# Optimization experiments

Hardware: AMD Instinct MI355X
Metric: run time of the kernel (lower is better)

Reference implementation:

```python
import jax, jax.numpy as jnp
import numpy as np

B, H, W, D, K = 64, 32, 32, 64, 512


def setup_inputs() -> dict:
    key = jax.random.key(0)
    k1, k2 = jax.random.split(key)
    x = jax.random.normal(k1, (B, H, W, D), dtype=jnp.float32)
    # tf.random_uniform_initializer default: U(-0.05, 0.05)
    embeddings = jax.random.uniform(k2, (D, K), dtype=jnp.float32,
                                    minval=-0.05, maxval=0.05)
    return {"x": x, "embeddings": embeddings}


def reference(x, embeddings):
    # embeddings: [D, K] (columns are codebook vectors)
    d = embeddings.shape[0]
    flat = x.reshape(-1, d)  # [N, D]
    # squared L2 distance to each code: ||z||^2 + ||e||^2 - 2 z.e
    distances = (jnp.sum(flat * flat, axis=1, keepdims=True)
                 + jnp.sum(embeddings * embeddings, axis=0)
                 - 2.0 * flat @ embeddings)  # [N, K]
    encoding_indices = jnp.argmin(distances, axis=1)  # [N]
    # one-hot @ embeddings^T  ==  gather of codebook rows
    quantized = jnp.take(embeddings.T, encoding_indices, axis=0).reshape(x.shape)
    sg = jax.lax.stop_gradient
    commitment_loss = jnp.mean((sg(quantized) - x) ** 2)  # commitment_cost = 1
    codebook_loss = jnp.mean((quantized - sg(x)) ** 2)
    loss = commitment_loss + codebook_loss
    out = x + sg(quantized - x)  # straight-through estimator
    return out, loss
```

## Files before the change

### kernel.cpp

```cpp
#include <hip/hip_runtime.h>

#define NVEC 65536
#define DIM 64
#define KCODES 512
#define VPB 128
#define NBLK 512
#define ELS 2048.0f
#define INV_ELS (1.0f / 2048.0f)
#define BIAS 8.0f
#define GAP_THR 2.5e-4f

typedef _Float16 f16x8 __attribute__((ext_vector_type(8)));
typedef float    f32x4 __attribute__((ext_vector_type(4)));
typedef unsigned long long u64;

#define WS_EN   4
#define WS_EH   1024
#define WS_EL   (1024 + 16384)
#define WS_PART 33792
#define WS_EMBT 34816

__global__ __launch_bounds__(512, 1) void prep_kernel(const float* __restrict__ emb,
                                                      float* __restrict__ ws) {
    const int tid = threadIdx.x;
    const int b   = blockIdx.x;
    if (b == 0) {
        float s = 0.f;
#pragma unroll
        for (int d = 0; d < DIM; ++d) { float v = emb[d * KCODES + tid]; s = fmaf(v, v, s); }
        ws[WS_EN + tid] = s;
    } else if (b <= 8) {
        const int fl = (b - 1) * 512 + tid;
        const int ct = fl >> 7, s5 = (fl >> 6) & 1, l = fl & 63;
        const int k  = ct * 16 + (l & 15);
        const int d0 = s5 * 32 + (l >> 4) * 8;
        f16x8 eh, el;
#pragma unroll
        for (int e = 0; e < 8; ++e) {
            float v = emb[(d0 + e) * KCODES + k];
            _Float16 h = (_Float16)v;
            _Float16 l16 = (_Float16)((v - (float)h) * ELS);
            eh[e] = -(h + h);
            el[e] = -(l16 + l16);
        }
        ((f16x8*)(ws + WS_EH))[fl] = eh;
        ((f16x8*)(ws + WS_EL))[fl] = el;
    } else {
        __shared__ float tl[64][65];
        const int kt = b - 9;
        const int r  = tid >> 3;
        const int g  = tid & 7;
#pragma unroll
        for (int i = 0; i < 8; ++i)
            tl[r][g * 8 + i] = emb[r * KCODES + kt * 64 + g * 8 + i];
        __syncthreads();
#pragma unroll
        for (int i = 0; i < 8; ++i)
            ws[WS_EMBT + (kt * 64 + r) * 64 + g * 8 + i] = tl[g * 8 + i][r];
    }
}

__global__ __launch_bounds__(512, 2) void vq_kernel(const float* __restrict__ x,
                                                    const float* __restrict__ ws_ro,
                                                    float* __restrict__ out,
                                                    float* __restrict__ part) {
    __shared__ f16x8 zhS[VPB][8];
    __shared__ f16x8 zlS[VPB][8];
    __shared__ float enS8[KCODES];
    __shared__ int   cand[VPB][2];
    __shared__ float sdfm[VPB][2];
    __shared__ float exd[VPB][2];
    __shared__ int   bksel[VPB];
    __shared__ float swl[8];

    const int tid  = threadIdx.x;
    const int wid  = tid >> 6;
    const int lane = tid & 63;
    const size_t xbase = (size_t)blockIdx.x * VPB * DIM;

    enS8[tid] = ws_ro[WS_EN + tid] + BIAS;

    {
        const int v  = tid >> 2;
        const int d0 = (tid & 3) * 16;
        const float* xp = x + xbase + v * DIM + d0;
        float4 a = *(const float4*)(xp);
        float4 b = *(const float4*)(xp + 4);
        float4 c = *(const float4*)(xp + 8);
        float4 e = *(const float4*)(xp + 12);
        float t0[8] = {a.x, a.y, a.z, a.w, b.x, b.y, b.z, b.w};
        float t1[8] = {c.x, c.y, c.z, c.w, e.x, e.y, e.z, e.w};
        f16x8 h0, l0, h1, l1;
#pragma unroll
        for (int i = 0; i < 8; ++i) {
            _Float16 h = (_Float16)t0[i]; h0[i] = h; l0[i] = (_Float16)((t0[i] - (float)h) * ELS);
            _Float16 g = (_Float16)t1[i]; h1[i] = g; l1[i] = (_Float16)((t1[i] - (float)g) * ELS);
        }
        const int u0 = ((d0 >> 3))     ^ (v & 7);
        const int u1 = ((d0 >> 3) + 1) ^ (v & 7);
        zhS[v][u0] = h0; zhS[v][u1] = h1;
        zlS[v][u0] = l0; zlS[v][u1] = l1;
    }
    __syncthreads();

    const int vb  = wid * 16;
    const int col = lane & 15;
    const int g4  = lane >> 4;
    const int vA  = vb + col;
    const int sw  = vA & 7;
    f16x8 ah0 = zhS[vA][(g4)     ^ sw];
    f16x8 ah1 = zhS[vA][(4 + g4) ^ sw];
    f16x8 al0 = zlS[vA][(g4)     ^ sw];
    f16x8 al1 = zlS[vA][(4 + g4) ^ sw];

    const f16x8* ehp = (const f16x8*)(ws_ro + WS_EH);
    const f16x8* elp = (const f16x8*)(ws_ro + WS_EL);

    unsigned b1[4] = {~0u, ~0u, ~0u, ~0u};
    unsigned b2[4] = {~0u, ~0u, ~0u, ~0u};

    f16x8 Ah0 = ehp[lane],        Ah1 = ehp[64 + lane];
    f16x8 Al0 = elp[lane],        Al1 = elp[64 + lane];
    f16x8 Bh0 = ehp[128 + lane],  Bh1 = ehp[192 + lane];
    f16x8 Bl0 = elp[128 + lane],  Bl1 = elp[192 + lane];
    int onx = 256 + lane;

#define COMPUTE(T, H0, H1, L0, L1) { \
        const float enk8 = enS8[(T) * 16 + col]; \
        f32x4 acch  = {enk8, enk8, enk8, enk8}; \
        f32x4 accm1 = {0.f, 0.f, 0.f, 0.f}; \
        f32x4 accm2 = {0.f, 0.f, 0.f, 0.f}; \
        acch  = __builtin_amdgcn_mfma_f32_16x16x32_f16(ah0, H0, acch,  0, 0, 0); \
        acch  = __builtin_amdgcn_mfma_f32_16x16x32_f16(ah1, H1, acch,  0, 0, 0); \
        accm1 = __builtin_amdgcn_mfma_f32_16x16x32_f16(al0, H0, accm1, 0, 0, 0); \
        accm1 = __builtin_amdgcn_mfma_f32_16x16x32_f16(ah0, L0, accm1, 0, 0, 0); \
        accm2 = __builtin_amdgcn_mfma_f32_16x16x32_f16(al1, H1, accm2, 0, 0, 0); \
        accm2 = __builtin_amdgcn_mfma_f32_16x16x32_f16(ah1, L1, accm2, 0, 0, 0); \
        _Pragma("unroll") \
        for (int j = 0; j < 4; ++j) { \
            float scb = fmaf(accm1[j] + accm2[j], INV_ELS, acch[j]); \
            unsigned u = (__float_as_uint(scb) & 0xFFFFFFE0u) | (unsigned)(T); \
            b2[j] = min(b2[j], max(u, b1[j])); \
            b1[j] = min(b1[j], u); \
        } }

#pragma unroll 1
    for (int ct = 0; ct < 32; ct += 2) {
        COMPUTE(ct, Ah0, Ah1, Al0, Al1)
        Ah0 = ehp[onx]; Ah1 = ehp[onx + 64];
        Al0 = elp[onx]; Al1 = elp[onx + 64];
        COMPUTE(ct + 1, Bh0, Bh1, Bl0, Bl1)
        Bh0 = ehp[onx + 128]; Bh1 = ehp[onx + 192];
        Bl0 = elp[onx + 128]; Bl1 = elp[onx + 192];
        onx += 256;
    }
#undef COMPUTE

    u64 q1[4], q2[4];
#pragma unroll
    for (int j = 0; j < 4; ++j) {
        q1[j] = ((u64)(b1[j] & 0xFFFFFFE0u) << 32) | (unsigned)((b1[j] & 31u) * 16 + col);
        q2[j] = ((u64)(b2[j] & 0xFFFFFFE0u) << 32) | (unsigned)((b2[j] & 31u) * 16 + col);
    }
#pragma unroll
    for (int m = 1; m <= 8; m <<= 1) {
#pragma unroll
        for (int j = 0; j < 4; ++j) {
            u64 qa = __shfl_xor(q1[j], m);
            u64 qb = __shfl_xor(q2[j], m);
            u64 lo = q1[j] < qa ? q1[j] : qa;
            u64 hi = q1[j] < qa ? qa : q1[j];
            u64 s2 = q2[j] < qb ? q2[j] : qb;
            q1[j] = lo;
            q2[j] = hi < s2 ? hi : s2;
        }
    }
    {
        const int j = lane & 15;
        if (j < 4) {
            const int v = vb + g4 * 4 + j;
            u64 s1 = j == 0 ? q1[0] : j == 1 ? q1[1] : j == 2 ? q1[2] : q1[3];
            u64 s2 = j == 0 ? q2[0] : j == 1 ? q2[1] : j == 2 ? q2[2] : q2[3];
            sdfm[v][0] = __uint_as_float((unsigned)(s1 >> 32));
            sdfm[v][1] = __uint_as_float((unsigned)(s2 >> 32));
            cand[v][0] = (int)(s1 & 0x1FFu);
            cand[v][1] = (int)(s2 & 0x1FFu);
        }
    }
    __syncthreads();

    if (tid < 2 * VPB) {
        const int v = tid >> 1, cc = tid & 1;
        float res = sdfm[v][cc];
        if (sdfm[v][1] - sdfm[v][0] <= GAP_THR) {
            const int k = cand[v][cc];
            const float* xr = x + xbase + v * DIM;
            const float* er = ws_ro + WS_EMBT + k * 64;
            float zn = 0.f, dot = 0.f;
#pragma unroll
            for (int d = 0; d < DIM; ++d) {
                float xv = xr[d];
                zn  = fmaf(xv, xv, zn);
                dot = fmaf(xv, er[d], dot);
            }
            res = fmaf(-2.0f, dot, zn + ws_ro[WS_EN + k]);
        }
        exd[v][cc] = res;
    }
    __syncthreads();
    if (tid < VPB) {
        const int k0 = cand[tid][0], k1 = cand[tid][1];
        const float d0 = exd[tid][0], d1 = exd[tid][1];
        const bool take2 = (d1 < d0) || (d1 == d0 && k1 < k0);
        bksel[tid] = take2 ? k1 : k0;
    }
    __syncthreads();

    const int v16 = tid >> 2;
    const int j16 = (tid & 3) * 16;
    const int bk  = bksel[v16];
    const int gvec = blockIdx.x * VPB + v16;
    const float*  xg  = x + (size_t)gvec * DIM + j16;
    float*        og  = out + (size_t)gvec * DIM + j16;
    const float4* et4 = (const float4*)(ws_ro + WS_EMBT + bk * 64);

    float lossLocal = 0.f;
#pragma unroll
    for (int c = 0; c < 4; ++c) {
        float4 q  = et4[(tid & 3) * 4 + c];
        *(float4*)(og + c * 4) = q;
        float4 xa = *(const float4*)(xg + c * 4);
        float a;
        a = q.x - xa.x; lossLocal = fmaf(a, a, lossLocal);
        a = q.y - xa.y; lossLocal = fmaf(a, a, lossLocal);
        a = q.z - xa.z; lossLocal = fmaf(a, a, lossLocal);
        a = q.w - xa.w; lossLocal = fmaf(a, a, lossLocal);
    }

#pragma unroll
    for (int off = 32; off; off >>= 1) lossLocal += __shfl_down(lossLocal, off, 64);
    if (lane == 0) swl[wid] = lossLocal;
    __syncthreads();
    if (tid == 0) {
        float s = 0.f;
#pragma unroll
        for (int i = 0; i < 8; ++i) s += swl[i];
        part[WS_PART + blockIdx.x] = s;
    }
}

__global__ __launch_bounds__(256, 1) void finish_kernel(const float* __restrict__ part,
                                                        float* __restrict__ out) {
    __shared__ float sw[4];
    const int tid = threadIdx.x, lane = tid & 63, wid = tid >> 6;
    float s = part[WS_PART + tid] + part[WS_PART + tid + 256];
#pragma unroll
    for (int off = 32; off; off >>= 1) s += __shfl_down(s, off, 64);
    if (lane == 0) sw[wid] = s;
    __syncthreads();
    if (tid == 0) {
        float total = sw[0] + sw[1] + sw[2] + sw[3];
        out[(size_t)NVEC * DIM] = 2.0f * total / (float)((size_t)NVEC * DIM);
    }
}

extern "C" void kernel_launch(void* const* d_in, const int* in_sizes, int n_in,
                              void* d_out, int out_size, void* d_ws, size_t ws_size,
                              hipStream_t stream) {
    const float* x   = (const float*)d_in[0];
    const float* emb = (const float*)d_in[1];
    float* out = (float*)d_out;
    float* ws  = (float*)d_ws;

    prep_kernel<<<dim3(17), dim3(512), 0, stream>>>(emb, ws);
    vq_kernel<<<dim3(NBLK), dim3(512), 0, stream>>>(x, ws, out, ws);
    finish_kernel<<<dim3(1), dim3(256), 0, stream>>>(ws, out);
}
```

Before: 39.11 us.

## Split codebook across wave pairs, each wave scoring 32 vectors

Each wave now handles 32 vectors against half of the codebook instead of 16 vectors against all 512 codes. Every loaded codebook fragment therefore feeds twice as many MFMAs, and the per-wave loop is half as long. A shared-memory merge step then combines the top-2 candidates from the two halves. Launch bounds are raised to 4 blocks per SM to target higher occupancy, at the cost of more registers per wave for the doubled fragments and accumulators, an extra barrier, and more shared memory.

```diff
diff --git a/kernel.cpp b/kernel.cpp
--- a/kernel.cpp
+++ b/kernel.cpp
@@ -60,13 +60,15 @@
     }
 }
 
-__global__ __launch_bounds__(512, 2) void vq_kernel(const float* __restrict__ x,
+__global__ __launch_bounds__(512, 4) void vq_kernel(const float* __restrict__ x,
                                                     const float* __restrict__ ws_ro,
                                                     float* __restrict__ out,
                                                     float* __restrict__ part) {
     __shared__ f16x8 zhS[VPB][8];
     __shared__ f16x8 zlS[VPB][8];
     __shared__ float enS8[KCODES];
+    __shared__ float sdf1[2][VPB], sdf2[2][VPB];
+    __shared__ int   k1a[2][VPB],  k2a[2][VPB];
     __shared__ int   cand[VPB][2];
     __shared__ float sdfm[VPB][2];
     __shared__ float exd[VPB][2];
@@ -103,89 +105,130 @@
     }
     __syncthreads();
 
-    const int vb  = wid * 16;
-    const int col = lane & 15;
-    const int g4  = lane >> 4;
-    const int vA  = vb + col;
-    const int sw  = vA & 7;
-    f16x8 ah0 = zhS[vA][(g4)     ^ sw];
-    f16x8 ah1 = zhS[vA][(4 + g4) ^ sw];
-    f16x8 al0 = zlS[vA][(g4)     ^ sw];
-    f16x8 al1 = zlS[vA][(4 + g4) ^ sw];
+    const int half = wid & 1;
+    const int vb   = (wid >> 1) * 32;
+    const int col  = lane & 15;
+    const int g4   = lane >> 4;
+    const int vA0  = vb + col,      sw0 = vA0 & 7;
+    const int vA1  = vb + 16 + col, sw1 = vA1 & 7;
+    f16x8 ah0_0 = zhS[vA0][(g4)     ^ sw0];
+    f16x8 ah1_0 = zhS[vA0][(4 + g4) ^ sw0];
+    f16x8 al0_0 = zlS[vA0][(g4)     ^ sw0];
+    f16x8 al1_0 = zlS[vA0][(4 + g4) ^ sw0];
+    f16x8 ah0_1 = zhS[vA1][(g4)     ^ sw1];
+    f16x8 ah1_1 = zhS[vA1][(4 + g4) ^ sw1];
+    f16x8 al0_1 = zlS[vA1][(g4)     ^ sw1];
+    f16x8 al1_1 = zlS[vA1][(4 + g4) ^ sw1];
 
     const f16x8* ehp = (const f16x8*)(ws_ro + WS_EH);
     const f16x8* elp = (const f16x8*)(ws_ro + WS_EL);
-
-    unsigned b1[4] = {~0u, ~0u, ~0u, ~0u};
-    unsigned b2[4] = {~0u, ~0u, ~0u, ~0u};
-
-    f16x8 Ah0 = ehp[lane],        Ah1 = ehp[64 + lane];
-    f16x8 Al0 = elp[lane],        Al1 = elp[64 + lane];
-    f16x8 Bh0 = ehp[128 + lane],  Bh1 = ehp[192 + lane];
-    f16x8 Bl0 = elp[128 + lane],  Bl1 = elp[192 + lane];
-    int onx = 256 + lane;
+    const int fb = half * 2048;
+
+    unsigned b1[8] = {~0u, ~0u, ~0u, ~0u, ~0u, ~0u, ~0u, ~0u};
+    unsigned b2[8] = {~0u, ~0u, ~0u, ~0u, ~0u, ~0u, ~0u, ~0u};
+
+    f16x8 Ah0 = ehp[fb + lane],        Ah1 = ehp[fb + 64 + lane];
+    f16x8 Al0 = elp[fb + lane],        Al1 = elp[fb + 64 + lane];
+    f16x8 Bh0 = ehp[fb + 128 + lane],  Bh1 = ehp[fb + 192 + lane];
+    f16x8 Bl0 = elp[fb + 128 + lane],  Bl1 = elp[fb + 192 + lane];
+    int onx = fb + 256 + lane;
 
 #define COMPUTE(T, H0, H1, L0, L1) { \
         const float enk8 = enS8[(T) * 16 + col]; \
-        f32x4 acch  = {enk8, enk8, enk8, enk8}; \
-        f32x4 accm1 = {0.f, 0.f, 0.f, 0.f}; \
-        f32x4 accm2 = {0.f, 0.f, 0.f, 0.f}; \
-        acch  = __builtin_amdgcn_mfma_f32_16x16x32_f16(ah0, H0, acch,  0, 0, 0); \
-        acch  = __builtin_amdgcn_mfma_f32_16x16x32_f16(ah1, H1, acch,  0, 0, 0); \
-        accm1 = __builtin_amdgcn_mfma_f32_16x16x32_f16(al0, H0, accm1, 0, 0, 0); \
-        accm1 = __builtin_amdgcn_mfma_f32_16x16x32_f16(ah0, L0, accm1, 0, 0, 0); \
-        accm2 = __builtin_amdgcn_mfma_f32_16x16x32_f16(al1, H1, accm2, 0, 0, 0); \
-        accm2 = __builtin_amdgcn_mfma_f32_16x16x32_f16(ah1, L1, accm2, 0, 0, 0); \
+        f32x4 acch0  = {enk8, enk8, enk8, enk8}; \
+        f32x4 accm0a = {0.f, 0.f, 0.f, 0.f}; \
+        f32x4 accm0b = {0.f, 0.f, 0.f, 0.f}; \
+        f32x4 acch1  = {enk8, enk8, enk8, enk8}; \
+        f32x4 accm1a = {0.f, 0.f, 0.f, 0.f}; \
+        f32x4 accm1b = {0.f, 0.f, 0.f, 0.f}; \
+        acch0  = __builtin_amdgcn_mfma_f32_16x16x32_f16(ah0_0, H0, acch0,  0, 0, 0); \
+        acch0  = __builtin_amdgcn_mfma_f32_16x16x32_f16(ah1_0, H1, acch0,  0, 0, 0); \
+        accm0a = __builtin_amdgcn_mfma_f32_16x16x32_f16(al0_0, H0, accm0a, 0, 0, 0); \
+        accm0a = __builtin_amdgcn_mfma_f32_16x16x32_f16(ah0_0, L0, accm0a, 0, 0, 0); \
+        accm0b = __builtin_amdgcn_mfma_f32_16x16x32_f16(al1_0, H1, accm0b, 0, 0, 0); \
+        accm0b = __builtin_amdgcn_mfma_f32_16x16x32_f16(ah1_0, L1, accm0b, 0, 0, 0); \
+        acch1  = __builtin_amdgcn_mfma_f32_16x16x32_f16(ah0_1, H0, acch1,  0, 0, 0); \
+        acch1  = __builtin_amdgcn_mfma_f32_16x16x32_f16(ah1_1, H1, acch1,  0, 0, 0); \
+        accm1a = __builtin_amdgcn_mfma_f32_16x16x32_f16(al0_1, H0, accm1a, 0, 0, 0); \
+        accm1a = __builtin_amdgcn_mfma_f32_16x16x32_f16(ah0_1, L0, accm1a, 0, 0, 0); \
+        accm1b = __builtin_amdgcn_mfma_f32_16x16x32_f16(al1_1, H1, accm1b, 0, 0, 0); \
+        accm1b = __builtin_amdgcn_mfma_f32_16x16x32_f16(ah1_1, L1, accm1b, 0, 0, 0); \
         _Pragma("unroll") \
         for (int j = 0; j < 4; ++j) { \
-            float scb = fmaf(accm1[j] + accm2[j], INV_ELS, acch[j]); \
+            float scb = fmaf(accm0a[j] + accm0b[j], INV_ELS, acch0[j]); \
             unsigned u = (__float_as_uint(scb) & 0xFFFFFFE0u) | (unsigned)(T); \
             b2[j] = min(b2[j], max(u, b1[j])); \
             b1[j] = min(b1[j], u); \
+            float scb1 = fmaf(accm1a[j] + accm1b[j], INV_ELS, acch1[j]); \
+            unsigned u1 = (__float_as_uint(scb1) & 0xFFFFFFE0u) | (unsigned)(T); \
+            b2[j + 4] = min(b2[j + 4], max(u1, b1[j + 4])); \
+            b1[j + 4] = min(b1[j + 4], u1); \
         } }
 
 #pragma unroll 1
-    for (int ct = 0; ct < 32; ct += 2) {
-        COMPUTE(ct, Ah0, Ah1, Al0, Al1)
+    for (int t = 0; t < 16; t += 2) {
+        COMPUTE(half * 16 + t, Ah0, Ah1, Al0, Al1)
         Ah0 = ehp[onx]; Ah1 = ehp[onx + 64];
         Al0 = elp[onx]; Al1 = elp[onx + 64];
-        COMPUTE(ct + 1, Bh0, Bh1, Bl0, Bl1)
+        COMPUTE(half * 16 + t + 1, Bh0, Bh1, Bl0, Bl1)
         Bh0 = ehp[onx + 128]; Bh1 = ehp[onx + 192];
         Bl0 = elp[onx + 128]; Bl1 = elp[onx + 192];
         onx += 256;
     }
 #undef COMPUTE
 
-    u64 q1[4], q2[4];
-#pragma unroll
-    for (int j = 0; j < 4; ++j) {
-        q1[j] = ((u64)(b1[j] & 0xFFFFFFE0u) << 32) | (unsigned)((b1[j] & 31u) * 16 + col);
-        q2[j] = ((u64)(b2[j] & 0xFFFFFFE0u) << 32) | (unsigned)((b2[j] & 31u) * 16 + col);
+    u64 q1[8], q2[8];
+#pragma unroll
+    for (int s = 0; s < 8; ++s) {
+        q1[s] = ((u64)(b1[s] & 0xFFFFFFE0u) << 32) | (unsigned)((b1[s] & 31u) * 16 + col);
+        q2[s] = ((u64)(b2[s] & 0xFFFFFFE0u) << 32) | (unsigned)((b2[s] & 31u) * 16 + col);
     }
 #pragma unroll
     for (int m = 1; m <= 8; m <<= 1) {
 #pragma unroll
-        for (int j = 0; j < 4; ++j) {
-            u64 qa = __shfl_xor(q1[j], m);
-            u64 qb = __shfl_xor(q2[j], m);
-            u64 lo = q1[j] < qa ? q1[j] : qa;
-            u64 hi = q1[j] < qa ? qa : q1[j];
-            u64 s2 = q2[j] < qb ? q2[j] : qb;
-            q1[j] = lo;
-            q2[j] = hi < s2 ? hi : s2;
+        for (int s = 0; s < 8; ++s) {
+            u64 qa = __shfl_xor(q1[s], m);
+            u64 qb = __shfl_xor(q2[s], m);
+            u64 lo = q1[s] < qa ? q1[s] : qa;
+            u64 hi = q1[s] < qa ? qa : q1[s];
+            u64 s2 = q2[s] < qb ? q2[s] : qb;
+            q1[s] = lo;
+            q2[s] = hi < s2 ? hi : s2;
         }
     }
     {
         const int j = lane & 15;
         if (j < 4) {
-            const int v = vb + g4 * 4 + j;
-            u64 s1 = j == 0 ? q1[0] : j == 1 ? q1[1] : j == 2 ? q1[2] : q1[3];
-            u64 s2 = j == 0 ? q2[0] : j == 1 ? q2[1] : j == 2 ? q2[2] : q2[3];
-            sdfm[v][0] = __uint_as_float((unsigned)(s1 >> 32));
-            sdfm[v][1] = __uint_as_float((unsigned)(s2 >> 32));
-            cand[v][0] = (int)(s1 & 0x1FFu);
-            cand[v][1] = (int)(s2 & 0x1FFu);
-        }
+            u64 s1a = j == 0 ? q1[0] : j == 1 ? q1[1] : j == 2 ? q1[2] : q1[3];
+            u64 s2a = j == 0 ? q2[0] : j == 1 ? q2[1] : j == 2 ? q2[2] : q2[3];
+            u64 s1b = j == 0 ? q1[4] : j == 1 ? q1[5] : j == 2 ? q1[6] : q1[7];
+            u64 s2b = j == 0 ? q2[4] : j == 1 ? q2[5] : j == 2 ? q2[6] : q2[7];
+            const int v0 = vb + g4 * 4 + j;
+            const int v1 = vb + 16 + g4 * 4 + j;
+            sdf1[half][v0] = __uint_as_float((unsigned)(s1a >> 32));
+            sdf2[half][v0] = __uint_as_float((unsigned)(s2a >> 32));
+            k1a[half][v0]  = (int)(s1a & 0x1FFu);
+            k2a[half][v0]  = (int)(s2a & 0x1FFu);
+            sdf1[half][v1] = __uint_as_float((unsigned)(s1b >> 32));
+            sdf2[half][v1] = __uint_as_float((unsigned)(s2b >> 32));
+            k1a[half][v1]  = (int)(s1b & 0x1FFu);
+            k2a[half][v1]  = (int)(s2b & 0x1FFu);
+        }
+    }
+    __syncthreads();
+
+    if (tid < VPB) {
+        const float a1 = sdf1[0][tid]; const int ka1 = k1a[0][tid];
+        const float a2 = sdf2[0][tid]; const int ka2 = k2a[0][tid];
+        const float c1 = sdf1[1][tid]; const int kc1 = k1a[1][tid];
+        const float c2 = sdf2[1][tid]; const int kc2 = k2a[1][tid];
+        const bool afirst = (a1 < c1) || (a1 == c1 && ka1 < kc1);
+        const float f1 = afirst ? a1 : c1;  const int fk1 = afirst ? ka1 : kc1;
+        const float u  = afirst ? a2 : c2;  const int uk  = afirst ? ka2 : kc2;
+        const float w  = afirst ? c1 : a1;  const int wk  = afirst ? kc1 : ka1;
+        const bool usec = (u < w) || (u == w && uk < wk);
+        cand[tid][0] = fk1;               sdfm[tid][0] = f1;
+        cand[tid][1] = usec ? uk : wk;    sdfm[tid][1] = usec ? u : w;
     }
     __syncthreads();
 
```

Measured after the change: 39.37 us. About the same (+0.7%).

## Load x fragments directly into MFMA registers and fold loss finish into last block

Applied to the files above, without the earlier changes.

Each lane now reads its own x row fragments from global memory and splits them into fp16 hi/lo registers directly, removing the shared-memory staging buffers and their barrier. The separate finish kernel is dropped: blocks publish partial sums, increment an atomic counter zeroed in the prep kernel, and the last block reduces all partials. This saves one kernel launch and some LDS traffic, at the cost of less coalesced x loads and an atomic plus fence at the end of each block.

```diff
diff --git a/kernel.cpp b/kernel.cpp
--- a/kernel.cpp
+++ b/kernel.cpp
@@ -25,6 +25,7 @@
     const int tid = threadIdx.x;
     const int b   = blockIdx.x;
     if (b == 0) {
+        if (tid == 0) ((unsigned*)ws)[0] = 0u;
         float s = 0.f;
 #pragma unroll
         for (int d = 0; d < DIM; ++d) { float v = emb[d * KCODES + tid]; s = fmaf(v, v, s); }
@@ -63,15 +64,14 @@
 __global__ __launch_bounds__(512, 2) void vq_kernel(const float* __restrict__ x,
                                                     const float* __restrict__ ws_ro,
                                                     float* __restrict__ out,
-                                                    float* __restrict__ part) {
-    __shared__ f16x8 zhS[VPB][8];
-    __shared__ f16x8 zlS[VPB][8];
+                                                    float* __restrict__ ws) {
     __shared__ float enS8[KCODES];
     __shared__ int   cand[VPB][2];
     __shared__ float sdfm[VPB][2];
     __shared__ float exd[VPB][2];
     __shared__ int   bksel[VPB];
     __shared__ float swl[8];
+    __shared__ int   lastFlag;
 
     const int tid  = threadIdx.x;
     const int wid  = tid >> 6;
@@ -80,38 +80,29 @@
 
     enS8[tid] = ws_ro[WS_EN + tid] + BIAS;
 
-    {
-        const int v  = tid >> 2;
-        const int d0 = (tid & 3) * 16;
-        const float* xp = x + xbase + v * DIM + d0;
-        float4 a = *(const float4*)(xp);
-        float4 b = *(const float4*)(xp + 4);
-        float4 c = *(const float4*)(xp + 8);
-        float4 e = *(const float4*)(xp + 12);
-        float t0[8] = {a.x, a.y, a.z, a.w, b.x, b.y, b.z, b.w};
-        float t1[8] = {c.x, c.y, c.z, c.w, e.x, e.y, e.z, e.w};
-        f16x8 h0, l0, h1, l1;
-#pragma unroll
-        for (int i = 0; i < 8; ++i) {
-            _Float16 h = (_Float16)t0[i]; h0[i] = h; l0[i] = (_Float16)((t0[i] - (float)h) * ELS);
-            _Float16 g = (_Float16)t1[i]; h1[i] = g; l1[i] = (_Float16)((t1[i] - (float)g) * ELS);
-        }
-        const int u0 = ((d0 >> 3))     ^ (v & 7);
-        const int u1 = ((d0 >> 3) + 1) ^ (v & 7);
-        zhS[v][u0] = h0; zhS[v][u1] = h1;
-        zlS[v][u0] = l0; zlS[v][u1] = l1;
-    }
-    __syncthreads();
-
     const int vb  = wid * 16;
     const int col = lane & 15;
     const int g4  = lane >> 4;
     const int vA  = vb + col;
-    const int sw  = vA & 7;
-    f16x8 ah0 = zhS[vA][(g4)     ^ sw];
-    f16x8 ah1 = zhS[vA][(4 + g4) ^ sw];
-    f16x8 al0 = zlS[vA][(g4)     ^ sw];
-    f16x8 al1 = zlS[vA][(4 + g4) ^ sw];
+    f16x8 ah0, al0, ah1, al1;
+    {
+        const float* xr = x + xbase + (size_t)vA * DIM + g4 * 8;
+        float4 q0 = *(const float4*)(xr);
+        float4 q1 = *(const float4*)(xr + 4);
+        float4 q2 = *(const float4*)(xr + 32);
+        float4 q3 = *(const float4*)(xr + 36);
+        float t0[8] = {q0.x, q0.y, q0.z, q0.w, q1.x, q1.y, q1.z, q1.w};
+        float t1[8] = {q2.x, q2.y, q2.z, q2.w, q3.x, q3.y, q3.z, q3.w};
+#pragma unroll
+        for (int i = 0; i < 8; ++i) {
+            _Float16 h = (_Float16)t0[i];
+            ah0[i] = h;
+            al0[i] = (_Float16)((t0[i] - (float)h) * ELS);
+            _Float16 g = (_Float16)t1[i];
+            ah1[i] = g;
+            al1[i] = (_Float16)((t1[i] - (float)g) * ELS);
+        }
+    }
 
     const f16x8* ehp = (const f16x8*)(ws_ro + WS_EH);
     const f16x8* elp = (const f16x8*)(ws_ro + WS_EL);
@@ -124,6 +115,8 @@
     f16x8 Bh0 = ehp[128 + lane],  Bh1 = ehp[192 + lane];
     f16x8 Bl0 = elp[128 + lane],  Bl1 = elp[192 + lane];
     int onx = 256 + lane;
+
+    __syncthreads();
 
 #define COMPUTE(T, H0, H1, L0, L1) { \
         const float enk8 = enS8[(T) * 16 + col]; \
@@ -245,22 +238,25 @@
         float s = 0.f;
 #pragma unroll
         for (int i = 0; i < 8; ++i) s += swl[i];
-        part[WS_PART + blockIdx.x] = s;
-    }
-}
-
-__global__ __launch_bounds__(256, 1) void finish_kernel(const float* __restrict__ part,
-                                                        float* __restrict__ out) {
-    __shared__ float sw[4];
-    const int tid = threadIdx.x, lane = tid & 63, wid = tid >> 6;
-    float s = part[WS_PART + tid] + part[WS_PART + tid + 256];
-#pragma unroll
-    for (int off = 32; off; off >>= 1) s += __shfl_down(s, off, 64);
-    if (lane == 0) sw[wid] = s;
-    __syncthreads();
-    if (tid == 0) {
-        float total = sw[0] + sw[1] + sw[2] + sw[3];
-        out[(size_t)NVEC * DIM] = 2.0f * total / (float)((size_t)NVEC * DIM);
+        ws[WS_PART + blockIdx.x] = s;
+        __threadfence();
+        unsigned prev = atomicAdd((unsigned*)ws, 1u);
+        lastFlag = (prev == (unsigned)(NBLK - 1)) ? 1 : 0;
+    }
+    __syncthreads();
+    if (lastFlag) {
+        __threadfence();
+        float s = ws[WS_PART + tid];
+#pragma unroll
+        for (int off = 32; off; off >>= 1) s += __shfl_down(s, off, 64);
+        if (lane == 0) swl[wid] = s;
+        __syncthreads();
+        if (tid == 0) {
+            float total = 0.f;
+#pragma unroll
+            for (int i = 0; i < 8; ++i) total += swl[i];
+            out[(size_t)NVEC * DIM] = 2.0f * total / (float)((size_t)NVEC * DIM);
+        }
     }
 }
 
@@ -274,5 +270,4 @@
 
     prep_kernel<<<dim3(17), dim3(512), 0, stream>>>(emb, ws);
     vq_kernel<<<dim3(NBLK), dim3(512), 0, stream>>>(x, ws, out, ws);
-    finish_kernel<<<dim3(1), dim3(256), 0, stream>>>(ws, out);
 }
```

After: 62.26 us. +59.2%, slower.
